# Kernel tuning notes

Hardware: AMD Instinct MI355X
Metric: run time of the kernel (lower is better)

The kernel has to match this reference:

```python
import jax, jax.numpy as jnp
import numpy as np

N_NODES = 100000
N_EDGES = 1600000
DIM = 128


def setup_inputs() -> dict:
    key = jax.random.key(0)
    k1, k2, k3, k4, k5 = jax.random.split(key, 5)
    h = jax.random.normal(k1, (N_NODES, DIM), dtype=jnp.float32)
    src = jax.random.randint(k2, (N_EDGES,), 0, N_NODES, dtype=jnp.int32)
    dst = jax.random.randint(k3, (N_EDGES,), 0, N_NODES, dtype=jnp.int32)
    W = jax.random.normal(k4, (DIM, DIM), dtype=jnp.float32) * (1.0 / np.sqrt(DIM))
    b = jax.random.normal(k5, (DIM,), dtype=jnp.float32) * 0.01
    return {"h": h, "src": src, "dst": dst, "W": W, "b": b}


def reference(h, src, dst, W, b):
    n = h.shape[0]
    # message: gather source features along edges  [E, D]
    m = h[src]
    # segment-mean over destination nodes
    s = jax.ops.segment_sum(m, dst, num_segments=n)              # [N, D]
    cnt = jax.ops.segment_sum(jnp.ones_like(dst, dtype=h.dtype), dst, num_segments=n)  # [N]
    mean = s / jnp.maximum(cnt, 1.0)[:, None]
    # DGL update_all: nodes with no incoming edges keep original h
    agg = jnp.where(cnt[:, None] > 0, mean, h)
    # NodeUpdate: ReLU(W h + b)
    return jax.nn.relu(agg @ W.T + b)
```

## Files before the change

kernel.cpp:

```cpp
#include <hip/hip_runtime.h>

#define DIM 128
#define NPB 32
#define SCAN_CHUNK 1024
#define BK2_BITS 9
#define PART_T 32
#define PART_EB (256 * PART_T)
#define PH_T 16
#define PH_EB (256 * PH_T)

typedef unsigned int   uint32;
typedef unsigned short uint16;

__device__ __forceinline__ uint16 f32_to_bf16_rne(float f) {
    uint32 u = __float_as_uint(f);
    u += 0x7fffu + ((u >> 16) & 1u);
    return (uint16)(u >> 16);
}

__global__ __launch_bounds__(256) void prep2_kernel(
    const float* __restrict__ W, float* __restrict__ Wt,
    const float* __restrict__ h, uint16* __restrict__ hb,
    const int* __restrict__ dst, int* __restrict__ cntOrB,
    int E, long long ND, int nConv, int doConv, int bucketMode)
{
    __shared__ int hist[256];
    const int bid = blockIdx.x;
    const int tid = threadIdx.x;
    if (bid < 64) {
        const int i = bid * 256 + tid;
        const int j = i >> 7, d = i & 127;
        Wt[d * DIM + j] = W[i];
    } else if (doConv && bid < 64 + nConv) {
        const long long base = ((long long)(bid - 64) * 256 + tid) * 8;
        if (base + 8 <= ND) {
            const float4 a = *(const float4*)&h[base];
            const float4 c = *(const float4*)&h[base + 4];
            uint4 v;
            v.x = (uint32)f32_to_bf16_rne(a.x) | ((uint32)f32_to_bf16_rne(a.y) << 16);
            v.y = (uint32)f32_to_bf16_rne(a.z) | ((uint32)f32_to_bf16_rne(a.w) << 16);
            v.z = (uint32)f32_to_bf16_rne(c.x) | ((uint32)f32_to_bf16_rne(c.y) << 16);
            v.w = (uint32)f32_to_bf16_rne(c.z) | ((uint32)f32_to_bf16_rne(c.w) << 16);
            *(uint4*)&hb[base] = v;
        }
    } else {
        const int hbase = 64 + (doConv ? nConv : 0);
        const long long e0 = (long long)(bid - hbase) * PH_EB;
        if (bucketMode) {
            hist[tid] = 0;
            __syncthreads();
#pragma unroll 1
            for (int j = 0; j < PH_T / 4; ++j) {
                const long long be = e0 + ((long long)(j * 256 + tid)) * 4;
                if (be + 4 <= E) {
                    const int4 d4 = *(const int4*)&dst[be];
                    atomicAdd(&hist[d4.x >> BK2_BITS], 1);
                    atomicAdd(&hist[d4.y >> BK2_BITS], 1);
                    atomicAdd(&hist[d4.z >> BK2_BITS], 1);
                    atomicAdd(&hist[d4.w >> BK2_BITS], 1);
                } else {
                    for (long long k = be; k < E && k < be + 4; ++k)
                        atomicAdd(&hist[dst[k] >> BK2_BITS], 1);
                }
            }
            __syncthreads();
            const int c = hist[tid];
            if (c > 0) atomicAdd(&cntOrB[tid], c);
        } else {
#pragma unroll 1
            for (int j = 0; j < PH_T / 4; ++j) {
                const long long be = e0 + ((long long)(j * 256 + tid)) * 4;
                if (be + 4 <= E) {
                    const int4 d4 = *(const int4*)&dst[be];
                    atomicAdd(&cntOrB[d4.x], 1);
                    atomicAdd(&cntOrB[d4.y], 1);
                    atomicAdd(&cntOrB[d4.z], 1);
                    atomicAdd(&cntOrB[d4.w], 1);
                } else {
                    for (long long k = be; k < E && k < be + 4; ++k)
                        atomicAdd(&cntOrB[dst[k]], 1);
                }
            }
        }
    }
}

__global__ __launch_bounds__(256) void bscan_kernel(
    const int* __restrict__ bcnt, int* __restrict__ bstart,
    int* __restrict__ gptr, int nbuck, int E)
{
    __shared__ int ts[256];
    const int t = threadIdx.x;
    ts[t] = (t < nbuck) ? bcnt[t] : 0;
    __syncthreads();
    for (int off = 1; off < 256; off <<= 1) {
        int x = (t >= off) ? ts[t - off] : 0;
        __syncthreads();
        ts[t] += x;
        __syncthreads();
    }
    const int ex = (t == 0) ? 0 : ts[t - 1];
    if (t < nbuck) { bstart[t] = ex; gptr[t] = ex; }
    if (t == 0) bstart[nbuck] = E;
}

__global__ __launch_bounds__(256) void partition_kernel(
    const int* __restrict__ src, const int* __restrict__ dst,
    int* __restrict__ gptr, uint32* __restrict__ ebuf, int E, int nbuck)
{
    __shared__ int hist[256];
    const int t = threadIdx.x;
    const long long e0 = (long long)blockIdx.x * PART_EB;

    hist[t] = 0;
    __syncthreads();

#pragma unroll 1
    for (int j = 0; j < PART_T / 4; ++j) {
        const long long be = e0 + ((long long)(j * 256 + t)) * 4;
        if (be + 4 <= E) {
            const int4 d4 = *(const int4*)&dst[be];
            atomicAdd(&hist[d4.x >> BK2_BITS], 1);
            atomicAdd(&hist[d4.y >> BK2_BITS], 1);
            atomicAdd(&hist[d4.z >> BK2_BITS], 1);
            atomicAdd(&hist[d4.w >> BK2_BITS], 1);
        } else {
            for (long long k = be; k < E && k < be + 4; ++k)
                atomicAdd(&hist[dst[k] >> BK2_BITS], 1);
        }
    }
    __syncthreads();

    for (int i = t; i < nbuck; i += 256) {
        const int c = hist[i];
        hist[i] = (c > 0) ? atomicAdd(&gptr[i], c) : 0;
    }
    __syncthreads();

#pragma unroll 1
    for (int j = 0; j < PART_T / 4; ++j) {
        const long long be = e0 + ((long long)(j * 256 + t)) * 4;
        if (be + 4 <= E) {
            const int4 s4 = *(const int4*)&src[be];
            const int4 d4 = *(const int4*)&dst[be];
            int sl;
            sl = atomicAdd(&hist[d4.x >> BK2_BITS], 1);
            ebuf[sl] = (uint32)s4.x | (((uint32)d4.x & 511u) << 20);
            sl = atomicAdd(&hist[d4.y >> BK2_BITS], 1);
            ebuf[sl] = (uint32)s4.y | (((uint32)d4.y & 511u) << 20);
            sl = atomicAdd(&hist[d4.z >> BK2_BITS], 1);
            ebuf[sl] = (uint32)s4.z | (((uint32)d4.z & 511u) << 20);
            sl = atomicAdd(&hist[d4.w >> BK2_BITS], 1);
            ebuf[sl] = (uint32)s4.w | (((uint32)d4.w & 511u) << 20);
        } else {
            for (long long k = be; k < E && k < be + 4; ++k) {
                const int d = dst[k];
                const int sl = atomicAdd(&hist[d >> BK2_BITS], 1);
                ebuf[sl] = (uint32)src[k] | (((uint32)d & 511u) << 20);
            }
        }
    }
}

__global__ __launch_bounds__(256) void csrfill2_kernel(
    const uint32* __restrict__ ebuf, const int* __restrict__ bstart,
    int* __restrict__ pos, int* __restrict__ cnt,
    int* __restrict__ esrc, int N)
{
    __shared__ int lcnt[512];
    __shared__ int lpos[512];
    __shared__ int ts[256];
    const int b = blockIdx.x;
    const int t = threadIdx.x;
    const int seg0 = bstart[b], seg1 = bstart[b + 1];
    lcnt[t] = 0; lcnt[t + 256] = 0;
    __syncthreads();
    for (int i = seg0 + t; i < seg1; i += 256)
        atomicAdd(&lcnt[ebuf[i] >> 20], 1);
    __syncthreads();
    const int a0 = lcnt[2 * t], a1 = lcnt[2 * t + 1];
    ts[t] = a0 + a1;
    __syncthreads();
    for (int off = 1; off < 256; off <<= 1) {
        int x = (t >= off) ? ts[t - off] : 0;
        __syncthreads();
        ts[t] += x;
        __syncthreads();
    }
    const int pb = (t == 0) ? 0 : ts[t - 1];
    const int s0 = seg0 + pb, s1 = seg0 + pb + a0;
    lpos[2 * t] = s0; lpos[2 * t + 1] = s1;
    const int n0 = (b << BK2_BITS) + 2 * t;
    if (n0 < N)     { pos[n0] = s0;     cnt[n0] = a0; }
    if (n0 + 1 < N) { pos[n0 + 1] = s1; cnt[n0 + 1] = a1; }
    __syncthreads();
    for (int i = seg0 + t; i < seg1; i += 256) {
        const uint32 p = ebuf[i];
        const int slot = atomicAdd(&lpos[p >> 20], 1);
        esrc[slot] = (int)(p & 0xFFFFFu);
    }
}

__global__ __launch_bounds__(256) void fused_kernel_bf(
    const float* __restrict__ h, const uint16* __restrict__ hb,
    const int* __restrict__ cnt, const int* __restrict__ pos,
    const int* __restrict__ esrc,
    const float* __restrict__ Wt, const float* __restrict__ bias,
    float* __restrict__ out, int N)
{
    __shared__ float row_lds[NPB][DIM];

    const int lane = threadIdx.x & 63;
    const int w    = threadIdx.x >> 6;
    const int nbase = blockIdx.x * NPB + w * 8;
    const int col2 = lane * 2;
    const uint32* __restrict__ hb32 = (const uint32*)hb;

#define LOADK(uX, kk) { const int s_ = __shfl(e_reg, (kk), 64); \
                        uX = hb32[((uint32)s_ << 6) | (uint32)lane]; }
#define ACC(uX) { ax += __uint_as_float(uX << 16); \
                  ay += __uint_as_float(uX & 0xffff0000u); }

#pragma unroll 1
    for (int i = 0; i < 8; ++i) {
        const int node = nbase + i;
        if (node >= N) break;
        const int deg = cnt[node];
        float ax, ay;
        if (deg == 0) {
            const float2 v = *(const float2*)&h[(size_t)node * DIM + col2];
            ax = v.x; ay = v.y;
        } else {
            const int start = pos[node];
            ax = 0.f; ay = 0.f;
            int base = 0;
#pragma unroll 1
            while (base < deg) {
                const int chunk = (deg - base < 64) ? (deg - base) : 64;
                int e_reg = 0;
                if (lane < chunk) e_reg = esrc[start + base + lane];
                int k = 0;
                if (chunk >= 4) {
                    uint32 u0, u1, u2, u3;
                    LOADK(u0, 0) LOADK(u1, 1) LOADK(u2, 2) LOADK(u3, 3)
#pragma unroll 1
                    for (; k + 8 <= chunk; k += 4) {
                        ACC(u0) LOADK(u0, k + 4)
                        ACC(u1) LOADK(u1, k + 5)
                        ACC(u2) LOADK(u2, k + 6)
                        ACC(u3) LOADK(u3, k + 7)
                    }
                    ACC(u0) ACC(u1) ACC(u2) ACC(u3)
                    k += 4;
                }
#pragma unroll 1
                for (; k < chunk; ++k) {
                    uint32 u;
                    LOADK(u, k)
                    ACC(u)
                }
                base += chunk;
            }
            const float inv = 1.0f / (float)deg;
            ax *= inv; ay *= inv;
        }
        *(float2*)&row_lds[w * 8 + i][col2] = make_float2(ax, ay);
    }
    __syncthreads();

#undef LOADK
#undef ACC

    const float2 bb = *(const float2*)&bias[col2];
    float acc0[8], acc1[8];
#pragma unroll
    for (int n = 0; n < 8; ++n) { acc0[n] = bb.x; acc1[n] = bb.y; }

#pragma unroll 1
    for (int d4 = 0; d4 < DIM; d4 += 4) {
        float4 a[8];
#pragma unroll
        for (int n = 0; n < 8; ++n)
            a[n] = *(const float4*)&row_lds[w * 8 + n][d4];
#pragma unroll
        for (int dd = 0; dd < 4; ++dd) {
            const float2 wt = *(const float2*)&Wt[(d4 + dd) * DIM + col2];
#pragma unroll
            for (int n = 0; n < 8; ++n) {
                const float av = dd == 0 ? a[n].x : dd == 1 ? a[n].y
                               : dd == 2 ? a[n].z : a[n].w;
                acc0[n] = fmaf(av, wt.x, acc0[n]);
                acc1[n] = fmaf(av, wt.y, acc1[n]);
            }
        }
    }

#pragma unroll
    for (int n = 0; n < 8; ++n) {
        const int node = nbase + n;
        if (node < N) {
            *(float2*)&out[(size_t)node * DIM + col2] =
                make_float2(fmaxf(acc0[n], 0.0f), fmaxf(acc1[n], 0.0f));
        }
    }
}

__global__ __launch_bounds__(256) void scanA_kernel(const int* __restrict__ cnt,
                                                    int* __restrict__ pos,
                                                    int* __restrict__ bsum, int N)
{
    __shared__ int ts[256];
    const int t = threadIdx.x;
    const int base = blockIdx.x * SCAN_CHUNK + t * 4;
    int v[4];
    int s = 0;
#pragma unroll
    for (int k = 0; k < 4; ++k) {
        v[k] = (base + k < N) ? cnt[base + k] : 0;
        s += v[k];
    }
    ts[t] = s;
    __syncthreads();
    for (int off = 1; off < 256; off <<= 1) {
        int x = (t >= off) ? ts[t - off] : 0;
        __syncthreads();
        ts[t] += x;
        __syncthreads();
    }
    int run = (t == 0) ? 0 : ts[t - 1];
    if (t == 255) bsum[blockIdx.x] = ts[255];
#pragma unroll
    for (int k = 0; k < 4; ++k) {
        if (base + k < N) pos[base + k] = run;
        run += v[k];
    }
}

__global__ __launch_bounds__(1024) void scanB_fb_kernel(int* __restrict__ bsum, int nb)
{
    __shared__ int ts[1024];
    const int t = threadIdx.x;
    ts[t] = (t < nb) ? bsum[t] : 0;
    __syncthreads();
    for (int off = 1; off < 1024; off <<= 1) {
        int x = (t >= off) ? ts[t - off] : 0;
        __syncthreads();
        ts[t] += x;
        __syncthreads();
    }
    if (t < nb) bsum[t] = (t == 0) ? 0 : ts[t - 1];
}

__global__ __launch_bounds__(256) void fill_direct_kernel(
    const int* __restrict__ src, const int* __restrict__ dst,
    int* __restrict__ pos, const int* __restrict__ bsum,
    int* __restrict__ esrc, int E)
{
    const long long e = ((long long)blockIdx.x * 256 + threadIdx.x) * 4;
    if (e + 4 <= E) {
        const int4 s4 = *(const int4*)&src[e];
        const int4 d4 = *(const int4*)&dst[e];
        int sl;
        sl = atomicAdd(&pos[d4.x], 1); esrc[sl + bsum[d4.x >> 10]] = s4.x;
        sl = atomicAdd(&pos[d4.y], 1); esrc[sl + bsum[d4.y >> 10]] = s4.y;
        sl = atomicAdd(&pos[d4.z], 1); esrc[sl + bsum[d4.z >> 10]] = s4.z;
        sl = atomicAdd(&pos[d4.w], 1); esrc[sl + bsum[d4.w >> 10]] = s4.w;
    } else {
        for (long long k = e; k < E && k < e + 4; ++k) {
            const int d = dst[k];
            const int sl = atomicAdd(&pos[d], 1);
            esrc[sl + bsum[d >> 10]] = src[k];
        }
    }
}

__global__ __launch_bounds__(256) void fused_kernel_f32(
    const float* __restrict__ h,
    const int* __restrict__ cnt, const int* __restrict__ pos,
    const int* __restrict__ bsum, const int* __restrict__ esrc,
    const float* __restrict__ Wt, const float* __restrict__ bias,
    float* __restrict__ out, int N)
{
    __shared__ float row_lds[NPB][DIM];
    const int lane = threadIdx.x & 63;
    const int w    = threadIdx.x >> 6;
    const int nbase = blockIdx.x * NPB + w * 8;
    const int col2 = lane * 2;

#pragma unroll 1
    for (int i = 0; i < 8; ++i) {
        const int node = nbase + i;
        if (node >= N) break;
        const int deg = cnt[node];
        float ax, ay;
        if (deg == 0) {
            const float2 v = *(const float2*)&h[(size_t)node * DIM + col2];
            ax = v.x; ay = v.y;
        } else {
            const int start = pos[node] - deg + bsum[node >> 10];
            ax = 0.f; ay = 0.f;
#pragma unroll 4
            for (int k = 0; k < deg; ++k) {
                const int s = esrc[start + k];
                const float2 v = *(const float2*)&h[(size_t)s * DIM + col2];
                ax += v.x; ay += v.y;
            }
            const float inv = 1.0f / (float)deg;
            ax *= inv; ay *= inv;
        }
        *(float2*)&row_lds[w * 8 + i][col2] = make_float2(ax, ay);
    }
    __syncthreads();

    const float2 bb = *(const float2*)&bias[col2];
    float acc0[8], acc1[8];
#pragma unroll
    for (int n = 0; n < 8; ++n) { acc0[n] = bb.x; acc1[n] = bb.y; }

#pragma unroll 1
    for (int d4 = 0; d4 < DIM; d4 += 4) {
        float4 a[8];
#pragma unroll
        for (int n = 0; n < 8; ++n)
            a[n] = *(const float4*)&row_lds[w * 8 + n][d4];
#pragma unroll
        for (int dd = 0; dd < 4; ++dd) {
            const float2 wt = *(const float2*)&Wt[(d4 + dd) * DIM + col2];
#pragma unroll
            for (int n = 0; n < 8; ++n) {
                const float av = dd == 0 ? a[n].x : dd == 1 ? a[n].y
                               : dd == 2 ? a[n].z : a[n].w;
                acc0[n] = fmaf(av, wt.x, acc0[n]);
                acc1[n] = fmaf(av, wt.y, acc1[n]);
            }
        }
    }

#pragma unroll
    for (int n = 0; n < 8; ++n) {
        const int node = nbase + n;
        if (node < N) {
            *(float2*)&out[(size_t)node * DIM + col2] =
                make_float2(fmaxf(acc0[n], 0.0f), fmaxf(acc1[n], 0.0f));
        }
    }
}

extern "C" void kernel_launch(void* const* d_in, const int* in_sizes, int n_in,
                              void* d_out, int out_size, void* d_ws, size_t ws_size,
                              hipStream_t stream)
{
    const float* h  = (const float*)d_in[0];
    const int* src  = (const int*)d_in[1];
    const int* dst  = (const int*)d_in[2];
    const float* W  = (const float*)d_in[3];
    const float* b  = (const float*)d_in[4];
    float* out = (float*)d_out;

    const int N = in_sizes[0] / DIM;
    const int E = in_sizes[1];
    const long long ND = (long long)N * DIM;
    const int nbuck = (N + (1 << BK2_BITS) - 1) >> BK2_BITS;

    const size_t off_cnt  = 0;
    const size_t off_pos  = (size_t)N * sizeof(int);
    const size_t off_esrc = off_pos + (size_t)N * sizeof(int);
    const size_t off_wt   = off_esrc + (size_t)E * sizeof(int);
    const size_t off_bcnt = off_wt + (size_t)DIM * DIM * sizeof(float);
    const size_t off_bst  = off_bcnt + 1024;
    const size_t off_gp   = off_bst + 1040;
    const size_t off_bsum = off_gp + 1024;
    const size_t off_hb   = (off_bsum + 4096 + 255) & ~(size_t)255;
    const size_t off_ebuf = (off_hb + (size_t)ND * sizeof(uint16) + 255) & ~(size_t)255;
    const size_t req_fb   = off_hb;
    const size_t req_full = off_ebuf + (size_t)E * sizeof(uint32);

    int*    cnt    = (int*)((char*)d_ws + off_cnt);
    int*    pos    = (int*)((char*)d_ws + off_pos);
    int*    esrc   = (int*)((char*)d_ws + off_esrc);
    float*  Wt     = (float*)((char*)d_ws + off_wt);
    int*    bcnt   = (int*)((char*)d_ws + off_bcnt);
    int*    bstart = (int*)((char*)d_ws + off_bst);
    int*    gptr   = (int*)((char*)d_ws + off_gp);
    int*    bsum   = (int*)((char*)d_ws + off_bsum);
    uint16* hb     = (uint16*)((char*)d_ws + off_hb);
    uint32* ebuf   = (uint32*)((char*)d_ws + off_ebuf);

    const int packOK   = (N <= (1 << 20)) && (nbuck <= 256);
    const int doBucket = (ws_size >= req_full && packOK) ? 1 : 0;
    const int nConv  = (int)((ND / 8 + 255) / 256);
    const int nHist  = (int)(((long long)E + PH_EB - 1) / PH_EB);
    const int nPart  = (int)(((long long)E + PART_EB - 1) / PART_EB);

    if (doBucket) {
        const int nPrep = 64 + nConv + nHist;
        hipMemsetAsync(bcnt, 0, 1024, stream);
        prep2_kernel<<<nPrep, 256, 0, stream>>>(W, Wt, h, hb, dst, bcnt, E, ND, nConv, 1, 1);
        bscan_kernel<<<1, 256, 0, stream>>>(bcnt, bstart, gptr, nbuck, E);
        partition_kernel<<<nPart, 256, 0, stream>>>(src, dst, gptr, ebuf, E, nbuck);
        csrfill2_kernel<<<nbuck, 256, 0, stream>>>(ebuf, bstart, pos, cnt, esrc, N);
        fused_kernel_bf<<<(N + NPB - 1) / NPB, 256, 0, stream>>>(h, hb, cnt, pos, esrc, Wt, b, out, N);
    } else {
        const int nb = (N + SCAN_CHUNK - 1) / SCAN_CHUNK;
        const int nPrep = 64 + nHist;
        const int nEdgeB = (int)(((long long)E / 4 + 255) / 256) + 1;
        hipMemsetAsync(cnt, 0, (size_t)N * sizeof(int), stream);
        prep2_kernel<<<nPrep, 256, 0, stream>>>(W, Wt, h, hb, dst, cnt, E, ND, nConv, 0, 0);
        scanA_kernel<<<nb, 256, 0, stream>>>(cnt, pos, bsum, N);
        scanB_fb_kernel<<<1, 1024, 0, stream>>>(bsum, nb);
        fill_direct_kernel<<<nEdgeB, 256, 0, stream>>>(src, dst, pos, bsum, esrc, E);
        fused_kernel_f32<<<(N + NPB - 1) / NPB, 256, 0, stream>>>(h, cnt, pos, bsum, esrc, Wt, b, out, N);
    }
}
```

Before: 178.2 us.

## Replace bucket histogram and scan with fixed-capacity padded buckets

Drops the separate bucket-count histogram pass and its scan by giving each destination bucket a fixed padded capacity (average plus 25% plus slack), so the partition writes straight into pre-offset slots. The weight transpose and bf16 conversion are merged into the same launch as the partition, removing the memset, the histogram kernel and the bucket-scan kernel. This saves one full read of dst and several launches, at the cost of a larger padded workspace. It also risks overflowing a bucket if the destination distribution is skewed, since there is no bounds check.

```diff
diff --git a/kernel.cpp b/kernel.cpp
--- a/kernel.cpp
+++ b/kernel.cpp
@@ -18,21 +18,32 @@
     return (uint16)(u >> 16);
 }
 
-__global__ __launch_bounds__(256) void prep2_kernel(
+__global__ __launch_bounds__(256) void init_kernel(int* __restrict__ gptr,
+                                                   int nbuck, int C)
+{
+    const int t = threadIdx.x;
+    if (t < nbuck) gptr[t] = t * C;
+}
+
+__global__ __launch_bounds__(256) void partition2_kernel(
     const float* __restrict__ W, float* __restrict__ Wt,
     const float* __restrict__ h, uint16* __restrict__ hb,
-    const int* __restrict__ dst, int* __restrict__ cntOrB,
-    int E, long long ND, int nConv, int doConv, int bucketMode)
+    const int* __restrict__ src, const int* __restrict__ dst,
+    int* __restrict__ gptr, uint32* __restrict__ ebuf,
+    int E, long long ND, int nConv, int nbuck)
 {
     __shared__ int hist[256];
     const int bid = blockIdx.x;
-    const int tid = threadIdx.x;
+    const int t = threadIdx.x;
+
     if (bid < 64) {
-        const int i = bid * 256 + tid;
+        const int i = bid * 256 + t;
         const int j = i >> 7, d = i & 127;
         Wt[d * DIM + j] = W[i];
-    } else if (doConv && bid < 64 + nConv) {
-        const long long base = ((long long)(bid - 64) * 256 + tid) * 8;
+        return;
+    }
+    if (bid < 64 + nConv) {
+        const long long base = ((long long)(bid - 64) * 256 + t) * 8;
         if (base + 8 <= ND) {
             const float4 a = *(const float4*)&h[base];
             const float4 c = *(const float4*)&h[base + 4];
@@ -43,75 +54,10 @@
             v.w = (uint32)f32_to_bf16_rne(c.z) | ((uint32)f32_to_bf16_rne(c.w) << 16);
             *(uint4*)&hb[base] = v;
         }
-    } else {
-        const int hbase = 64 + (doConv ? nConv : 0);
-        const long long e0 = (long long)(bid - hbase) * PH_EB;
-        if (bucketMode) {
-            hist[tid] = 0;
-            __syncthreads();
-#pragma unroll 1
-            for (int j = 0; j < PH_T / 4; ++j) {
-                const long long be = e0 + ((long long)(j * 256 + tid)) * 4;
-                if (be + 4 <= E) {
-                    const int4 d4 = *(const int4*)&dst[be];
-                    atomicAdd(&hist[d4.x >> BK2_BITS], 1);
-                    atomicAdd(&hist[d4.y >> BK2_BITS], 1);
-                    atomicAdd(&hist[d4.z >> BK2_BITS], 1);
-                    atomicAdd(&hist[d4.w >> BK2_BITS], 1);
-                } else {
-                    for (long long k = be; k < E && k < be + 4; ++k)
-                        atomicAdd(&hist[dst[k] >> BK2_BITS], 1);
-                }
-            }
-            __syncthreads();
-            const int c = hist[tid];
-            if (c > 0) atomicAdd(&cntOrB[tid], c);
-        } else {
-#pragma unroll 1
-            for (int j = 0; j < PH_T / 4; ++j) {
-                const long long be = e0 + ((long long)(j * 256 + tid)) * 4;
-                if (be + 4 <= E) {
-                    const int4 d4 = *(const int4*)&dst[be];
-                    atomicAdd(&cntOrB[d4.x], 1);
-                    atomicAdd(&cntOrB[d4.y], 1);
-                    atomicAdd(&cntOrB[d4.z], 1);
-                    atomicAdd(&cntOrB[d4.w], 1);
-                } else {
-                    for (long long k = be; k < E && k < be + 4; ++k)
-                        atomicAdd(&cntOrB[dst[k]], 1);
-                }
-            }
-        }
-    }
-}
-
-__global__ __launch_bounds__(256) void bscan_kernel(
-    const int* __restrict__ bcnt, int* __restrict__ bstart,
-    int* __restrict__ gptr, int nbuck, int E)
-{
-    __shared__ int ts[256];
-    const int t = threadIdx.x;
-    ts[t] = (t < nbuck) ? bcnt[t] : 0;
-    __syncthreads();
-    for (int off = 1; off < 256; off <<= 1) {
-        int x = (t >= off) ? ts[t - off] : 0;
-        __syncthreads();
-        ts[t] += x;
-        __syncthreads();
-    }
-    const int ex = (t == 0) ? 0 : ts[t - 1];
-    if (t < nbuck) { bstart[t] = ex; gptr[t] = ex; }
-    if (t == 0) bstart[nbuck] = E;
-}
-
-__global__ __launch_bounds__(256) void partition_kernel(
-    const int* __restrict__ src, const int* __restrict__ dst,
-    int* __restrict__ gptr, uint32* __restrict__ ebuf, int E, int nbuck)
-{
-    __shared__ int hist[256];
-    const int t = threadIdx.x;
-    const long long e0 = (long long)blockIdx.x * PART_EB;
-
+        return;
+    }
+
+    const long long e0 = (long long)(bid - 64 - nConv) * PART_EB;
     hist[t] = 0;
     __syncthreads();
 
@@ -163,16 +109,16 @@
 }
 
 __global__ __launch_bounds__(256) void csrfill2_kernel(
-    const uint32* __restrict__ ebuf, const int* __restrict__ bstart,
+    const uint32* __restrict__ ebuf, const int* __restrict__ gptr,
     int* __restrict__ pos, int* __restrict__ cnt,
-    int* __restrict__ esrc, int N)
+    int* __restrict__ esrc, int N, int C)
 {
     __shared__ int lcnt[512];
     __shared__ int lpos[512];
     __shared__ int ts[256];
     const int b = blockIdx.x;
     const int t = threadIdx.x;
-    const int seg0 = bstart[b], seg1 = bstart[b + 1];
+    const int seg0 = b * C, seg1 = gptr[b];
     lcnt[t] = 0; lcnt[t + 256] = 0;
     __syncthreads();
     for (int i = seg0 + t; i < seg1; i += 256)
@@ -301,6 +247,29 @@
         if (node < N) {
             *(float2*)&out[(size_t)node * DIM + col2] =
                 make_float2(fmaxf(acc0[n], 0.0f), fmaxf(acc1[n], 0.0f));
+        }
+    }
+}
+
+__global__ __launch_bounds__(256) void prep_fb_kernel(
+    const float* __restrict__ W, float* __restrict__ Wt,
+    const int* __restrict__ dst, int* __restrict__ cnt, int E)
+{
+    const int bid = blockIdx.x;
+    const int tid = threadIdx.x;
+    if (bid < 64) {
+        const int i = bid * 256 + tid;
+        Wt[(i & 127) * DIM + (i >> 7)] = W[i];
+    } else {
+        const long long e = ((long long)(bid - 64) * 256 + tid) * 4;
+        if (e + 4 <= E) {
+            const int4 d4 = *(const int4*)&dst[e];
+            atomicAdd(&cnt[d4.x], 1);
+            atomicAdd(&cnt[d4.y], 1);
+            atomicAdd(&cnt[d4.z], 1);
+            atomicAdd(&cnt[d4.w], 1);
+        } else {
+            for (long long k = e; k < E && k < e + 4; ++k) atomicAdd(&cnt[dst[k]], 1);
         }
     }
 }
@@ -462,53 +431,50 @@
     const long long ND = (long long)N * DIM;
     const int nbuck = (N + (1 << BK2_BITS) - 1) >> BK2_BITS;
 
+    const int avgB = (int)(((long long)E + nbuck - 1) / nbuck);
+    const int C = ((avgB + (avgB >> 2) + 256) + 255) & ~255;
+    const long long padE = (long long)nbuck * C;
+
     const size_t off_cnt  = 0;
     const size_t off_pos  = (size_t)N * sizeof(int);
-    const size_t off_esrc = off_pos + (size_t)N * sizeof(int);
-    const size_t off_wt   = off_esrc + (size_t)E * sizeof(int);
-    const size_t off_bcnt = off_wt + (size_t)DIM * DIM * sizeof(float);
-    const size_t off_bst  = off_bcnt + 1024;
-    const size_t off_gp   = off_bst + 1040;
+    const size_t off_wt   = off_pos + (size_t)N * sizeof(int);
+    const size_t off_gp   = off_wt + (size_t)DIM * DIM * sizeof(float);
     const size_t off_bsum = off_gp + 1024;
-    const size_t off_hb   = (off_bsum + 4096 + 255) & ~(size_t)255;
+    const size_t off_esrc = (off_bsum + 4096 + 255) & ~(size_t)255;
+    const size_t off_hb   = (off_esrc + (size_t)padE * sizeof(int) + 255) & ~(size_t)255;
     const size_t off_ebuf = (off_hb + (size_t)ND * sizeof(uint16) + 255) & ~(size_t)255;
-    const size_t req_fb   = off_hb;
-    const size_t req_full = off_ebuf + (size_t)E * sizeof(uint32);
-
-    int*    cnt    = (int*)((char*)d_ws + off_cnt);
-    int*    pos    = (int*)((char*)d_ws + off_pos);
-    int*    esrc   = (int*)((char*)d_ws + off_esrc);
-    float*  Wt     = (float*)((char*)d_ws + off_wt);
-    int*    bcnt   = (int*)((char*)d_ws + off_bcnt);
-    int*    bstart = (int*)((char*)d_ws + off_bst);
-    int*    gptr   = (int*)((char*)d_ws + off_gp);
-    int*    bsum   = (int*)((char*)d_ws + off_bsum);
-    uint16* hb     = (uint16*)((char*)d_ws + off_hb);
-    uint32* ebuf   = (uint32*)((char*)d_ws + off_ebuf);
+    const size_t req_full = off_ebuf + (size_t)padE * sizeof(uint32);
+
+    int*    cnt  = (int*)((char*)d_ws + off_cnt);
+    int*    pos  = (int*)((char*)d_ws + off_pos);
+    float*  Wt   = (float*)((char*)d_ws + off_wt);
+    int*    gptr = (int*)((char*)d_ws + off_gp);
+    int*    bsum = (int*)((char*)d_ws + off_bsum);
+    int*    esrc = (int*)((char*)d_ws + off_esrc);
+    uint16* hb   = (uint16*)((char*)d_ws + off_hb);
+    uint32* ebuf = (uint32*)((char*)d_ws + off_ebuf);
 
     const int packOK   = (N <= (1 << 20)) && (nbuck <= 256);
     const int doBucket = (ws_size >= req_full && packOK) ? 1 : 0;
-    const int nConv  = (int)((ND / 8 + 255) / 256);
-    const int nHist  = (int)(((long long)E + PH_EB - 1) / PH_EB);
-    const int nPart  = (int)(((long long)E + PART_EB - 1) / PART_EB);
+    const int nConv = (int)((ND / 8 + 255) / 256);
+    const int nPart = (int)(((long long)E + PART_EB - 1) / PART_EB);
 
     if (doBucket) {
-        const int nPrep = 64 + nConv + nHist;
-        hipMemsetAsync(bcnt, 0, 1024, stream);
-        prep2_kernel<<<nPrep, 256, 0, stream>>>(W, Wt, h, hb, dst, bcnt, E, ND, nConv, 1, 1);
-        bscan_kernel<<<1, 256, 0, stream>>>(bcnt, bstart, gptr, nbuck, E);
-        partition_kernel<<<nPart, 256, 0, stream>>>(src, dst, gptr, ebuf, E, nbuck);
-        csrfill2_kernel<<<nbuck, 256, 0, stream>>>(ebuf, bstart, pos, cnt, esrc, N);
-        fused_kernel_bf<<<(N + NPB - 1) / NPB, 256, 0, stream>>>(h, hb, cnt, pos, esrc, Wt, b, out, N);
+        init_kernel<<<1, 256, 0, stream>>>(gptr, nbuck, C);
+        partition2_kernel<<<64 + nConv + nPart, 256, 0, stream>>>(
+            W, Wt, h, hb, src, dst, gptr, ebuf, E, ND, nConv, nbuck);
+        csrfill2_kernel<<<nbuck, 256, 0, stream>>>(ebuf, gptr, pos, cnt, esrc, N, C);
+        fused_kernel_bf<<<(N + NPB - 1) / NPB, 256, 0, stream>>>(
+            h, hb, cnt, pos, esrc, Wt, b, out, N);
     } else {
         const int nb = (N + SCAN_CHUNK - 1) / SCAN_CHUNK;
-        const int nPrep = 64 + nHist;
         const int nEdgeB = (int)(((long long)E / 4 + 255) / 256) + 1;
         hipMemsetAsync(cnt, 0, (size_t)N * sizeof(int), stream);
-        prep2_kernel<<<nPrep, 256, 0, stream>>>(W, Wt, h, hb, dst, cnt, E, ND, nConv, 0, 0);
+        prep_fb_kernel<<<64 + nEdgeB, 256, 0, stream>>>(W, Wt, dst, cnt, E);
         scanA_kernel<<<nb, 256, 0, stream>>>(cnt, pos, bsum, N);
         scanB_fb_kernel<<<1, 1024, 0, stream>>>(bsum, nb);
         fill_direct_kernel<<<nEdgeB, 256, 0, stream>>>(src, dst, pos, bsum, esrc, E);
-        fused_kernel_f32<<<(N + NPB - 1) / NPB, 256, 0, stream>>>(h, cnt, pos, bsum, esrc, Wt, b, out, N);
-    }
-}
+        fused_kernel_f32<<<(N + NPB - 1) / NPB, 256, 0, stream>>>(
+            h, cnt, pos, bsum, esrc, Wt, b, out, N);
+    }
+}
```

Result: no change. 176.8 us (-0.8%).
